# Optimization experiments

Hardware: AMD Instinct MI355X
Metric: run time of the kernel (lower is better)

Reference implementation:

```python
import jax, jax.numpy as jnp
import numpy as np

# MoE config (matches init_kwargs)
E = 32      # num_experts
K = 4       # num_experts_per_tok (top_k)
H = 1024    # hidden_size
I = 512     # moe_intermediate_size (shared expert uses I * num_shared_experts = I)
B, S = 2, 2048
T = B * S
C = 1024
ROUTED_SCALE = 1.0


def _silu_and_mul(gu):
    g, u = jnp.split(gu, 2, axis=-1)
    return jax.nn.silu(g) * u


def setup_inputs() -> dict:
    key = jax.random.key(0)
    ks = jax.random.split(key, 6)
    s = 0.02
    return {
        "hidden_states": jax.random.normal(ks[0], (B, S, H), jnp.float32),
        "gate_w": jax.random.normal(ks[1], (E, H), jnp.float32) * s,
        "w_gate_up": jax.random.normal(ks[2], (E, H, 2 * I), jnp.float32) * s,
        "w_down": jax.random.normal(ks[3], (E, I, H), jnp.float32) * s,
        "shared_w_gate_up": jax.random.normal(ks[4], (H, 2 * I), jnp.float32) * s,
        "shared_w_down": jax.random.normal(ks[5], (I, H), jnp.float32) * s,
    }


def reference(hidden_states, gate_w, w_gate_up, w_down, shared_w_gate_up, shared_w_down):
    b, s, h = hidden_states.shape
    x = hidden_states.reshape(-1, h)                      # [T, H]
    t = x.shape[0]

    # --- router: gate linear -> softmax -> top-k -> renormalize ---
    logits = x @ gate_w.T                                 # [T, E]
    probs = jax.nn.softmax(logits, axis=-1)
    topk_w, topk_idx = jax.lax.top_k(probs, K)            # [T, K]
    topk_w = topk_w / jnp.sum(topk_w, axis=-1, keepdims=True)  # norm_topk_prob
    topk_w = topk_w * ROUTED_SCALE

    # --- dispatch: sort (token, slot) assignments by expert, scatter into capacity buffer ---
    e_flat = topk_idx.reshape(-1)                         # [T*K]
    w_flat = topk_w.reshape(-1)
    t_flat = jnp.repeat(jnp.arange(t), K)
    order = jnp.argsort(e_flat)                           # stable sort by expert id
    e_s, w_s, t_s = e_flat[order], w_flat[order], t_flat[order]
    counts = jax.ops.segment_sum(jnp.ones_like(e_s), e_s, num_segments=E)
    starts = jnp.cumsum(counts) - counts                  # exclusive prefix sum
    pos = jnp.arange(t * K) - starts[e_s]                 # position within expert group
    slot = jnp.minimum(pos, C)                            # overflow -> trash slot C
    buf = jnp.zeros((E, C + 1, h), x.dtype).at[e_s, slot].set(x[t_s])

    # --- grouped expert MLP (silu-gated) ---
    gu = jnp.einsum('ech,ehi->eci', buf[:, :C], w_gate_up)        # [E, C, 2I]
    expert_out = jnp.einsum('eci,eih->ech', _silu_and_mul(gu), w_down)  # [E, C, H]
    expert_out = jnp.pad(expert_out, ((0, 0), (0, 1), (0, 0)))    # trash slot reads zero

    # --- combine: gather back, weight, scatter-add per token ---
    gate = jnp.where(pos < C, w_s, 0.0)[:, None]
    routed = jnp.zeros_like(x).at[t_s].add(expert_out[e_s, slot] * gate)

    # --- shared expert MLP ---
    shared = _silu_and_mul(x @ shared_w_gate_up) @ shared_w_down

    return (routed + shared).reshape(b, s, h)
```

## Files before the change

kernel.cpp:

```cpp
#include <hip/hip_runtime.h>
#include <cstdint>
#include <cstddef>

#define NEXP   32
#define TOPK   4
#define HD     1024
#define ID     512
#define TT     4096
#define CAP    1024
#define SHARED_BASE (NEXP*CAP)
#define NSLOT  (NEXP*CAP + TT)
#define MAXTILES 320

#define KSPLIT 16
#define KCH    64
#define KSUB   16

typedef __attribute__((ext_vector_type(4))) float f32x4;
typedef __bf16 bf16x8 __attribute__((ext_vector_type(8)));

__device__ __forceinline__ unsigned short f2bf(float f) {
    union { float f; unsigned int u; } v; v.f = f;
    unsigned int u = v.u;
    u = (u + 0x7FFFu + ((u >> 16) & 1u)) >> 16;
    return (unsigned short)u;
}
__device__ __forceinline__ float bf2f(unsigned short s) {
    union { unsigned int u; float f; } v; v.u = ((unsigned int)s) << 16;
    return v.f;
}

#define GLOAD_LDS16(g, l)                                                     \
    __builtin_amdgcn_global_load_lds(                                         \
        (__attribute__((address_space(1))) void*)(g),                         \
        (__attribute__((address_space(3))) void*)(l), 16, 0, 0)

__global__ __launch_bounds__(256)
void k_prep(const float* __restrict__ wgu, const float* __restrict__ sgu,
            const float* __restrict__ wdn, const float* __restrict__ sdn,
            unsigned short* __restrict__ wgup_b, unsigned short* __restrict__ wdn_b,
            const float* __restrict__ x, const float* __restrict__ gw,
            float* __restrict__ part, unsigned short* __restrict__ xb) {
    __shared__ __align__(16) char smem[18944];
    const int z = blockIdx.z;
    const int tid = threadIdx.x;

    if (z < 66) {
        const float* s; unsigned short* d;
        const int lb = blockIdx.y * 16 + blockIdx.x;
        if (z < 33) {
            s = (z < NEXP) ? wgu + (size_t)z * (1024 * 1024) : sgu;
            d = wgup_b + (size_t)z * (1024 * 1024);
        } else {
            if (lb >= 128) return;
            int zz = z - 33;
            s = (zz < NEXP) ? wdn + (size_t)zz * (512 * 1024) : sdn;
            d = wdn_b + (size_t)zz * (512 * 1024);
        }
        const size_t base = (size_t)lb * 1024;
#pragma unroll
        for (int j = 0; j < 4; j++) {
            size_t i = base + j * 256 + tid;
            float4 v = ((const float4*)s)[i];
            ushort4 o;
            o.x = f2bf(v.x); o.y = f2bf(v.y); o.z = f2bf(v.z); o.w = f2bf(v.w);
            ((ushort4*)d)[i] = o;
        }
        return;
    }

    float (*xsT)[260] = reinterpret_cast<float(*)[260]>(smem);
    float (*gsT)[36]  = reinterpret_cast<float(*)[36]>(smem + KSUB * 260 * 4);
    const int lane = tid & 63, wv = tid >> 6;
    const int tg = lane >> 2, eg = lane & 3;
    const int t0 = blockIdx.x * 256;
    const int kbase = blockIdx.y * KCH;
    const int tbase = wv * 64 + tg * 4;
    const int ebase = eg * 8;

    float acc[4][8];
#pragma unroll
    for (int j = 0; j < 4; j++)
#pragma unroll
        for (int i = 0; i < 8; i++) acc[j][i] = 0.f;

    for (int ks = 0; ks < KCH; ks += KSUB) {
        const int k0 = kbase + ks;
        if (ks > 0) __syncthreads();
#pragma unroll
        for (int p = 0; p < 4; p++) {
            int vid = p * 256 + tid;
            int t = vid >> 2, kq = (vid & 3) * 4;
            float4 v = *(const float4*)(x + (size_t)(t0 + t) * HD + k0 + kq);
            xsT[kq + 0][t] = v.x; xsT[kq + 1][t] = v.y;
            xsT[kq + 2][t] = v.z; xsT[kq + 3][t] = v.w;
            ushort4 o;
            o.x = f2bf(v.x); o.y = f2bf(v.y); o.z = f2bf(v.z); o.w = f2bf(v.w);
            *(ushort4*)(xb + (size_t)(t0 + t) * HD + k0 + kq) = o;
        }
#pragma unroll
        for (int p = 0; p < 2; p++) {
            int vid = p * 256 + tid;
            int e = vid >> 4, k = vid & 15;
            gsT[k][e] = gw[(size_t)e * HD + k0 + k];
        }
        __syncthreads();
#pragma unroll 4
        for (int k = 0; k < KSUB; k++) {
            float4 xv = *(const float4*)&xsT[k][tbase];
            float4 g0 = *(const float4*)&gsT[k][ebase];
            float4 g1 = *(const float4*)&gsT[k][ebase + 4];
            float xa[4] = {xv.x, xv.y, xv.z, xv.w};
#pragma unroll
            for (int j = 0; j < 4; j++) {
                acc[j][0] += xa[j] * g0.x; acc[j][1] += xa[j] * g0.y;
                acc[j][2] += xa[j] * g0.z; acc[j][3] += xa[j] * g0.w;
                acc[j][4] += xa[j] * g1.x; acc[j][5] += xa[j] * g1.y;
                acc[j][6] += xa[j] * g1.z; acc[j][7] += xa[j] * g1.w;
            }
        }
    }
    const size_t base = ((size_t)blockIdx.y * TT + (t0 + tbase)) * 32 + ebase;
#pragma unroll
    for (int j = 0; j < 4; j++) {
        float4 w0, w1;
        w0.x = acc[j][0]; w0.y = acc[j][1]; w0.z = acc[j][2]; w0.w = acc[j][3];
        w1.x = acc[j][4]; w1.y = acc[j][5]; w1.z = acc[j][6]; w1.w = acc[j][7];
        *(float4*)(part + base + (size_t)j * 32) = w0;
        *(float4*)(part + base + (size_t)j * 32 + 4) = w1;
    }
}

__global__ __launch_bounds__(256)
void k_topk(const float* __restrict__ part,
            int* __restrict__ choice, float* __restrict__ cw,
            int* __restrict__ tok, float* __restrict__ wgt) {
    const int lane = threadIdx.x & 63, wv = threadIdx.x >> 6;
    const int t = blockIdx.x * 4 + wv;
    const int e = lane & 31;
    const int sbase = (lane >> 5) * 8;
    float v = 0.f;
#pragma unroll
    for (int s = 0; s < 8; s++)
        v += part[((size_t)(sbase + s) * TT + t) * 32 + e];
    v += __shfl_xor(v, 32);
    float sc = (lane < 32) ? v : -INFINITY;

    float lv[TOPK]; int le[TOPK];
#pragma unroll
    for (int r = 0; r < TOPK; r++) {
        float m = sc;
#pragma unroll
        for (int d = 1; d < 64; d <<= 1) m = fmaxf(m, __shfl_xor(m, d));
        unsigned long long ball = __ballot(sc == m);
        int widx = __ffsll(ball) - 1;
        lv[r] = m; le[r] = widx;
        if (lane == widx) sc = -INFINITY;
    }
    if (lane == 0) {
        float wv4[TOPK], wsum = 0.f;
#pragma unroll
        for (int r = 0; r < TOPK; r++) { wv4[r] = __expf(lv[r] - lv[0]); wsum += wv4[r]; }
#pragma unroll
        for (int r = 0; r < TOPK; r++) {
            choice[t * TOPK + r] = le[r];
            cw[t * TOPK + r] = wv4[r] / wsum;
        }
        tok[SHARED_BASE + t] = t;
        wgt[SHARED_BASE + t] = 1.0f;
    }
}

__global__ __launch_bounds__(1024)
void k_assign(const int* __restrict__ choice, const float* __restrict__ cw,
              int* __restrict__ cnt, int* __restrict__ tok,
              float* __restrict__ wgt, int* __restrict__ smap) {
    const int e = blockIdx.x;
    const int tid = threadIdx.x, lane = tid & 63, wv = tid >> 6;
    __shared__ int wtot[16];
    int running = 0;
    for (int it = 0; it < TT / 1024; it++) {
        const int t = it * 1024 + tid;
        const int4   c4 = *(const int4*)(choice + t * 4);
        const float4 w4 = *(const float4*)(cw + t * 4);
        unsigned m = (unsigned)(c4.x == e) | ((unsigned)(c4.y == e) << 1)
                   | ((unsigned)(c4.z == e) << 2) | ((unsigned)(c4.w == e) << 3);
        int mc = __popc(m);
        int pre = mc;
#pragma unroll
        for (int d = 1; d < 64; d <<= 1) {
            int up = __shfl_up(pre, d);
            if (lane >= d) pre += up;
        }
        if (lane == 63) wtot[wv] = pre;
        const int wpre = pre - mc;
        __syncthreads();
        int woff = 0, tot = 0;
#pragma unroll
        for (int w = 0; w < 16; w++) { int c = wtot[w]; tot += c; if (w < wv) woff += c; }
        int base = running + woff + wpre;
        running += tot;
        __syncthreads();
        if (m) {
            const float wa[4] = {w4.x, w4.y, w4.z, w4.w};
            int k = 0;
#pragma unroll
            for (int r = 0; r < 4; r++) {
                if (m & (1u << r)) {
                    int pos = base + k;
                    int i = t * 4 + r;
                    if (pos < CAP) {
                        int slot = e * CAP + pos;
                        tok[slot] = t;
                        wgt[slot] = wa[r];
                        smap[i] = slot;
                    } else {
                        smap[i] = -1;
                    }
                    k++;
                }
            }
        }
    }
    if (tid == 0) cnt[e] = min(running, CAP);
}

template <int KD, bool GATHER, bool SILU>
__global__ __launch_bounds__(256)
void k_moe_gemm(const unsigned short* __restrict__ Ab,
                const unsigned short* __restrict__ Bt,
                unsigned short* __restrict__ Cout,
                const int* __restrict__ tok,
                const int* __restrict__ cnt) {
    const int tid  = threadIdx.x;
    const int lane = tid & 63;
    const int wv   = tid >> 6;

    int c_l = (lane < NEXP) ? min(cnt[lane], CAP) : ((lane == NEXP) ? TT : 0);
    int nt_l = (c_l + 127) >> 7;
    int pre = nt_l;
#pragma unroll
    for (int d = 1; d < 64; d <<= 1) {
        int up = __shfl_up(pre, d);
        if (lane >= d) pre += up;
    }
    const int ntl = __shfl(pre, 63);
    const int chunk = (ntl + 7) >> 3;
    const int c_xcd = blockIdx.x;
    const int qy = blockIdx.y;
    if ((qy >> 3) >= chunk) return;
    const int j = c_xcd * chunk + (qy >> 3);
    if (j >= ntl) return;
    const int nt = qy & 7;
    const int start_l = pre - nt_l;
    const bool mine = (j >= start_l) && (j < start_l + nt_l);
    const unsigned long long bl = __ballot(mine);
    const int e_lane = __ffsll((long long)bl) - 1;
    const int e  = e_lane;
    const int mt = j - __shfl(start_l, e_lane);
    const int cE = __shfl(c_l, e_lane);

    const int slotbase = (e < NEXP) ? e * CAP : SHARED_BASE;
    const int m0 = mt * 128;
    const int rowsv = min(128, cE - m0);

    const unsigned short* Bte = Bt + (size_t)e * ((size_t)KD * 1024);

    __shared__ unsigned short As[3][128 * 32];
    __shared__ unsigned short Bs[2][128 * 32];

    const int rr   = lane >> 2;
    const int segA = (lane & 3) ^ ((lane >> 4) & 3);
    const int r0 = wv * 32 + rr;
    const int r1 = r0 + 16;

    int ga0 = m0 + r0, ga1 = m0 + r1;
    int ra0, ra1;
    if (GATHER) {
        ra0 = (ga0 < cE) ? tok[slotbase + ga0] : 0;
        ra1 = (ga1 < cE) ? tok[slotbase + ga1] : 0;
    } else {
        ra0 = slotbase + ga0;
        ra1 = slotbase + ga1;
    }
    const unsigned short* ap0 = Ab + (size_t)ra0 * KD + segA * 8;
    const unsigned short* ap1 = Ab + (size_t)ra1 * KD + segA * 8;
    const int aoff0 = (wv * 32) * 32, aoff1 = (wv * 32 + 16) * 32;

    const int hB = lane >> 5;
    const int nw = lane & 31;
    int rB[4], offB[4];
    int bcol;
    if (SILU) {
        const int sn0 = nw * 4;
        const int side = sn0 >> 6;
        const int jj0 = sn0 & 63;
        bcol = (side ? 512 : 0) + nt * 64 + jj0;
#pragma unroll
        for (int q = 0; q < 4; q++) {
            int jj = jj0 + q;
            rB[q] = ((jj >> 5) << 6) + (side << 5) + (jj & 31);
        }
    } else {
        bcol = nt * 128 + nw * 4;
#pragma unroll
        for (int q = 0; q < 4; q++) rB[q] = nw * 4 + q;
    }
#pragma unroll
    for (int q = 0; q < 4; q++) {
        int slot = wv ^ ((rB[q] >> 2) & 3);
        offB[q] = rB[q] * 32 + slot * 8 + hB * 4;
    }
    const unsigned short* bp = Bte + (size_t)(wv * 8 + hB * 4) * 1024 + bcol;

#define BLOAD(IT, R0, R1, R2, R3)                                             \
    {                                                                         \
        const unsigned short* bpk = bp + (size_t)(IT) * 32 * 1024;            \
        R0 = *(const uint2*)(bpk);                                            \
        R1 = *(const uint2*)(bpk + 1024);                                     \
        R2 = *(const uint2*)(bpk + 2048);                                     \
        R3 = *(const uint2*)(bpk + 3072);                                     \
    }
#define BPACK(BUF, R0, R1, R2, R3)                                            \
    {                                                                         \
        unsigned short* bw = &Bs[BUF][0];                                     \
        _Pragma("unroll")                                                     \
        for (int q = 0; q < 4; q++) {                                         \
            unsigned e0 = ((q < 2 ? R0.x : R0.y) >> (16 * (q & 1))) & 0xffffu;\
            unsigned e1 = ((q < 2 ? R1.x : R1.y) >> (16 * (q & 1))) & 0xffffu;\
            unsigned e2 = ((q < 2 ? R2.x : R2.y) >> (16 * (q & 1))) & 0xffffu;\
            unsigned e3 = ((q < 2 ? R3.x : R3.y) >> (16 * (q & 1))) & 0xffffu;\
            uint2 wv2; wv2.x = e0 | (e1 << 16); wv2.y = e2 | (e3 << 16);      \
            *(uint2*)(bw + offB[q]) = wv2;                                    \
        }                                                                     \
    }

    f32x4 acc[4][4];
#pragma unroll
    for (int i = 0; i < 4; i++)
#pragma unroll
        for (int j2 = 0; j2 < 4; j2++) acc[i][j2] = (f32x4)(0.0f);

    const int mrow = lane & 15;
    const int quad = lane >> 4;
    const int wm = wv >> 1, wn = wv & 1;
    const int sw = (quad ^ ((mrow >> 2) & 3)) * 8;

    const int aRdOff = (wm * 64 + mrow) * 32 + sw;
    const int bRdOff = (wn * 64 + mrow) * 32 + sw;

    uint2 rb0, rb1, rb2, rb3;
    BLOAD(0, rb0, rb1, rb2, rb3);
    __builtin_amdgcn_sched_barrier(0);
    GLOAD_LDS16(ap0, As[0] + aoff0);
    GLOAD_LDS16(ap1, As[0] + aoff1);
    GLOAD_LDS16(ap0 + 32, As[1] + aoff0);
    GLOAD_LDS16(ap1 + 32, As[1] + aoff1);
    __builtin_amdgcn_sched_barrier(0);
    BPACK(0, rb0, rb1, rb2, rb3);

    const int NIT = KD / 32;
    int pA = 0, pB = 0;
    for (int it = 0; it < NIT; ++it) {
        asm volatile("s_waitcnt vmcnt(2) lgkmcnt(0)" ::: "memory");
        __builtin_amdgcn_s_barrier();
        asm volatile("" ::: "memory");

        const bool hasB = (it + 1) < NIT;
        const bool hasA = (it + 2) < NIT;
        if (hasB) BLOAD(it + 1, rb0, rb1, rb2, rb3);
        __builtin_amdgcn_sched_barrier(0);
        if (hasA) {
            int pw = pA + 2; if (pw >= 3) pw -= 3;
            GLOAD_LDS16(ap0 + (it + 2) * 32, As[pw] + aoff0);
            GLOAD_LDS16(ap1 + (it + 2) * 32, As[pw] + aoff1);
        }
        __builtin_amdgcn_sched_barrier(0);

        bf16x8 af[4], bf[4];
#pragma unroll
        for (int i = 0; i < 4; i++) {
            af[i] = *(const bf16x8*)(As[pA] + aRdOff + i * 16 * 32);
            bf[i] = *(const bf16x8*)(Bs[pB] + bRdOff + i * 16 * 32);
        }
#pragma unroll
        for (int mi = 0; mi < 4; mi++)
#pragma unroll
            for (int nj = 0; nj < 4; nj++)
                acc[mi][nj] = __builtin_amdgcn_mfma_f32_16x16x32_bf16(
                    af[mi], bf[nj], acc[mi][nj], 0, 0, 0);
        __builtin_amdgcn_sched_barrier(0);
        if (hasB) BPACK(pB ^ 1, rb0, rb1, rb2, rb3);

        pA++; if (pA >= 3) pA = 0;
        pB ^= 1;
    }
#undef BLOAD
#undef BPACK

    if (SILU) {
#pragma unroll
        for (int mi = 0; mi < 4; mi++)
#pragma unroll
            for (int nj = 0; nj < 2; nj++) {
                f32x4 g = acc[mi][nj];
                f32x4 u = acc[mi][nj + 2];
#pragma unroll
                for (int r = 0; r < 4; r++) {
                    int rloc = wm * 64 + mi * 16 + quad * 4 + r;
                    if (rloc < rowsv) {
                        float gv = g[r], uv = u[r];
                        float a = (gv / (1.f + __expf(-gv))) * uv;
                        int c = nt * 64 + wn * 32 + nj * 16 + mrow;
                        Cout[(size_t)(slotbase + m0 + rloc) * ID + c] = f2bf(a);
                    }
                }
            }
    } else {
#pragma unroll
        for (int mi = 0; mi < 4; mi++)
#pragma unroll
            for (int nj = 0; nj < 4; nj++) {
                f32x4 v = acc[mi][nj];
#pragma unroll
                for (int r = 0; r < 4; r++) {
                    int rloc = wm * 64 + mi * 16 + quad * 4 + r;
                    if (rloc < rowsv) {
                        int c = nt * 128 + wn * 64 + nj * 16 + mrow;
                        Cout[(size_t)(slotbase + m0 + rloc) * HD + c] = f2bf(v[r]);
                    }
                }
            }
    }
}

__global__ __launch_bounds__(256)
void k_combine(const unsigned short* __restrict__ eout,
               const int* __restrict__ smap,
               const float* __restrict__ wgt,
               float* __restrict__ out) {
    const int t = blockIdx.x;
    const int h0 = threadIdx.x * 4;
    ushort4 q = *(const ushort4*)(eout + (size_t)(SHARED_BASE + t) * HD + h0);
    float a0 = bf2f(q.x), a1 = bf2f(q.y), a2 = bf2f(q.z), a3 = bf2f(q.w);
#pragma unroll
    for (int r = 0; r < TOPK; r++) {
        int slot = smap[t * TOPK + r];
        if (slot >= 0) {
            float w = wgt[slot];
            ushort4 e4 = *(const ushort4*)(eout + (size_t)slot * HD + h0);
            a0 += w * bf2f(e4.x); a1 += w * bf2f(e4.y);
            a2 += w * bf2f(e4.z); a3 += w * bf2f(e4.w);
        }
    }
    float4 o; o.x = a0; o.y = a1; o.z = a2; o.w = a3;
    *(float4*)(out + (size_t)t * HD + h0) = o;
}

extern "C" void kernel_launch(void* const* d_in, const int* in_sizes, int n_in,
                              void* d_out, int out_size, void* d_ws, size_t ws_size,
                              hipStream_t stream) {
    const float* x   = (const float*)d_in[0];
    const float* gw  = (const float*)d_in[1];
    const float* wgu = (const float*)d_in[2];
    const float* wdn = (const float*)d_in[3];
    const float* sgu = (const float*)d_in[4];
    const float* sdn = (const float*)d_in[5];
    float* out = (float*)d_out;

    char* w = (char*)d_ws;
    size_t off = 0;
    int* cnt = (int*)(w + off);                       off += 256;
    unsigned short* xb     = (unsigned short*)(w + off); off += (size_t)TT * HD * 2;
    unsigned short* wgup_b = (unsigned short*)(w + off); off += (size_t)33 * 1024 * 1024 * 2;
    unsigned short* wdn_b  = (unsigned short*)(w + off); off += (size_t)33 * 512 * 1024 * 2;
    unsigned short* act    = (unsigned short*)(w + off); off += (size_t)NSLOT * ID * 2;
    int*   tok    = (int*)(w + off);   off += (size_t)NSLOT * 4;
    float* wgt    = (float*)(w + off); off += (size_t)NSLOT * 4;
    int*   smap   = (int*)(w + off);   off += (size_t)TT * TOPK * 4;
    int*   choice = (int*)(w + off);   off += (size_t)TT * TOPK * 4;
    float* cw     = (float*)(w + off); off += (size_t)TT * TOPK * 4;

    float* part = (float*)act;
    unsigned short* eout = xb;

    k_prep<<<dim3(16, 16, 67), 256, 0, stream>>>(wgu, sgu, wdn, sdn,
                                                 wgup_b, wdn_b, x, gw, part, xb);
    k_topk<<<TT / 4, 256, 0, stream>>>(part, choice, cw, tok, wgt);
    k_assign<<<NEXP, 1024, 0, stream>>>(choice, cw, cnt, tok, wgt, smap);

    k_moe_gemm<1024, true, true><<<dim3(8, MAXTILES), 256, 0, stream>>>(xb, wgup_b, act, tok, cnt);
    k_moe_gemm<512, false, false><<<dim3(8, MAXTILES), 256, 0, stream>>>(act, wdn_b, eout, tok, cnt);

    k_combine<<<TT, 256, 0, stream>>>(eout, smap, wgt, out);
}
```

Before: 440.7 us.

## Fuse fp32-to-bf16 weight conversion into MoE GEMM B-tile loads

Removes the separate pass that converts all expert and shared weights to bf16 in a workspace. The grouped GEMMs now read fp32 weights directly and convert them to bf16 with packed convert instructions while staging B tiles into shared memory. This saves writing and re-reading about 100MB of bf16 weights. In exchange, each GEMM tile reads twice as many weight bytes, and weights are re-read per M-tile, which raises global traffic when experts have several tiles. Expert outputs get their own buffer instead of aliasing xb.

```diff
diff --git a/kernel.cpp b/kernel.cpp
--- a/kernel.cpp
+++ b/kernel.cpp
@@ -36,41 +36,11 @@
         (__attribute__((address_space(3))) void*)(l), 16, 0, 0)
 
 __global__ __launch_bounds__(256)
-void k_prep(const float* __restrict__ wgu, const float* __restrict__ sgu,
-            const float* __restrict__ wdn, const float* __restrict__ sdn,
-            unsigned short* __restrict__ wgup_b, unsigned short* __restrict__ wdn_b,
-            const float* __restrict__ x, const float* __restrict__ gw,
-            float* __restrict__ part, unsigned short* __restrict__ xb) {
-    __shared__ __align__(16) char smem[18944];
-    const int z = blockIdx.z;
+void k_logits(const float* __restrict__ x, const float* __restrict__ gw,
+              float* __restrict__ part, unsigned short* __restrict__ xb) {
+    __shared__ float xsT[KSUB][260];
+    __shared__ float gsT[KSUB][36];
     const int tid = threadIdx.x;
-
-    if (z < 66) {
-        const float* s; unsigned short* d;
-        const int lb = blockIdx.y * 16 + blockIdx.x;
-        if (z < 33) {
-            s = (z < NEXP) ? wgu + (size_t)z * (1024 * 1024) : sgu;
-            d = wgup_b + (size_t)z * (1024 * 1024);
-        } else {
-            if (lb >= 128) return;
-            int zz = z - 33;
-            s = (zz < NEXP) ? wdn + (size_t)zz * (512 * 1024) : sdn;
-            d = wdn_b + (size_t)zz * (512 * 1024);
-        }
-        const size_t base = (size_t)lb * 1024;
-#pragma unroll
-        for (int j = 0; j < 4; j++) {
-            size_t i = base + j * 256 + tid;
-            float4 v = ((const float4*)s)[i];
-            ushort4 o;
-            o.x = f2bf(v.x); o.y = f2bf(v.y); o.z = f2bf(v.z); o.w = f2bf(v.w);
-            ((ushort4*)d)[i] = o;
-        }
-        return;
-    }
-
-    float (*xsT)[260] = reinterpret_cast<float(*)[260]>(smem);
-    float (*gsT)[36]  = reinterpret_cast<float(*)[36]>(smem + KSUB * 260 * 4);
     const int lane = tid & 63, wv = tid >> 6;
     const int tg = lane >> 2, eg = lane & 3;
     const int t0 = blockIdx.x * 256;
@@ -228,7 +198,8 @@
 template <int KD, bool GATHER, bool SILU>
 __global__ __launch_bounds__(256)
 void k_moe_gemm(const unsigned short* __restrict__ Ab,
-                const unsigned short* __restrict__ Bt,
+                const float* __restrict__ Bf,
+                const float* __restrict__ BfS,
                 unsigned short* __restrict__ Cout,
                 const int* __restrict__ tok,
                 const int* __restrict__ cnt) {
@@ -264,7 +235,7 @@
     const int m0 = mt * 128;
     const int rowsv = min(128, cE - m0);
 
-    const unsigned short* Bte = Bt + (size_t)e * ((size_t)KD * 1024);
+    const float* Btf = (e < NEXP) ? Bf + (size_t)e * ((size_t)KD * 1024) : BfS;
 
     __shared__ unsigned short As[3][128 * 32];
     __shared__ unsigned short Bs[2][128 * 32];
@@ -311,26 +282,32 @@
         int slot = wv ^ ((rB[q] >> 2) & 3);
         offB[q] = rB[q] * 32 + slot * 8 + hB * 4;
     }
-    const unsigned short* bp = Bte + (size_t)(wv * 8 + hB * 4) * 1024 + bcol;
-
-#define BLOAD(IT, R0, R1, R2, R3)                                             \
+    const float* bpf = Btf + (size_t)(wv * 8 + hB * 4) * 1024 + bcol;
+
+    float4 F0, F1, F2, F3;
+#define BLOAD(IT)                                                             \
     {                                                                         \
-        const unsigned short* bpk = bp + (size_t)(IT) * 32 * 1024;            \
-        R0 = *(const uint2*)(bpk);                                            \
-        R1 = *(const uint2*)(bpk + 1024);                                     \
-        R2 = *(const uint2*)(bpk + 2048);                                     \
-        R3 = *(const uint2*)(bpk + 3072);                                     \
-    }
-#define BPACK(BUF, R0, R1, R2, R3)                                            \
+        const float* bpk = bpf + (size_t)(IT) * 32 * 1024;                    \
+        F0 = *(const float4*)(bpk);                                           \
+        F1 = *(const float4*)(bpk + 1024);                                    \
+        F2 = *(const float4*)(bpk + 2048);                                    \
+        F3 = *(const float4*)(bpk + 3072);                                    \
+    }
+#define BPACK(BUF)                                                            \
     {                                                                         \
         unsigned short* bw = &Bs[BUF][0];                                     \
+        const float* a0p = (const float*)&F0;                                 \
+        const float* a1p = (const float*)&F1;                                 \
+        const float* a2p = (const float*)&F2;                                 \
+        const float* a3p = (const float*)&F3;                                 \
         _Pragma("unroll")                                                     \
         for (int q = 0; q < 4; q++) {                                         \
-            unsigned e0 = ((q < 2 ? R0.x : R0.y) >> (16 * (q & 1))) & 0xffffu;\
-            unsigned e1 = ((q < 2 ? R1.x : R1.y) >> (16 * (q & 1))) & 0xffffu;\
-            unsigned e2 = ((q < 2 ? R2.x : R2.y) >> (16 * (q & 1))) & 0xffffu;\
-            unsigned e3 = ((q < 2 ? R3.x : R3.y) >> (16 * (q & 1))) & 0xffffu;\
-            uint2 wv2; wv2.x = e0 | (e1 << 16); wv2.y = e2 | (e3 << 16);      \
+            unsigned lo, hi;                                                  \
+            asm("v_cvt_pk_bf16_f32 %0, %1, %2"                                \
+                : "=v"(lo) : "v"(a0p[q]), "v"(a1p[q]));                       \
+            asm("v_cvt_pk_bf16_f32 %0, %1, %2"                                \
+                : "=v"(hi) : "v"(a2p[q]), "v"(a3p[q]));                       \
+            uint2 wv2; wv2.x = lo; wv2.y = hi;                                \
             *(uint2*)(bw + offB[q]) = wv2;                                    \
         }                                                                     \
     }
@@ -349,15 +326,14 @@
     const int aRdOff = (wm * 64 + mrow) * 32 + sw;
     const int bRdOff = (wn * 64 + mrow) * 32 + sw;
 
-    uint2 rb0, rb1, rb2, rb3;
-    BLOAD(0, rb0, rb1, rb2, rb3);
+    BLOAD(0);
     __builtin_amdgcn_sched_barrier(0);
     GLOAD_LDS16(ap0, As[0] + aoff0);
     GLOAD_LDS16(ap1, As[0] + aoff1);
     GLOAD_LDS16(ap0 + 32, As[1] + aoff0);
     GLOAD_LDS16(ap1 + 32, As[1] + aoff1);
     __builtin_amdgcn_sched_barrier(0);
-    BPACK(0, rb0, rb1, rb2, rb3);
+    BPACK(0);
 
     const int NIT = KD / 32;
     int pA = 0, pB = 0;
@@ -368,7 +344,7 @@
 
         const bool hasB = (it + 1) < NIT;
         const bool hasA = (it + 2) < NIT;
-        if (hasB) BLOAD(it + 1, rb0, rb1, rb2, rb3);
+        if (hasB) BLOAD(it + 1);
         __builtin_amdgcn_sched_barrier(0);
         if (hasA) {
             int pw = pA + 2; if (pw >= 3) pw -= 3;
@@ -390,7 +366,7 @@
                 acc[mi][nj] = __builtin_amdgcn_mfma_f32_16x16x32_bf16(
                     af[mi], bf[nj], acc[mi][nj], 0, 0, 0);
         __builtin_amdgcn_sched_barrier(0);
-        if (hasB) BPACK(pB ^ 1, rb0, rb1, rb2, rb3);
+        if (hasB) BPACK(pB ^ 1);
 
         pA++; if (pA >= 3) pA = 0;
         pB ^= 1;
@@ -471,10 +447,9 @@
     char* w = (char*)d_ws;
     size_t off = 0;
     int* cnt = (int*)(w + off);                       off += 256;
-    unsigned short* xb     = (unsigned short*)(w + off); off += (size_t)TT * HD * 2;
-    unsigned short* wgup_b = (unsigned short*)(w + off); off += (size_t)33 * 1024 * 1024 * 2;
-    unsigned short* wdn_b  = (unsigned short*)(w + off); off += (size_t)33 * 512 * 1024 * 2;
-    unsigned short* act    = (unsigned short*)(w + off); off += (size_t)NSLOT * ID * 2;
+    unsigned short* xb   = (unsigned short*)(w + off); off += (size_t)TT * HD * 2;
+    unsigned short* act  = (unsigned short*)(w + off); off += (size_t)NSLOT * ID * 2;
+    unsigned short* eout = (unsigned short*)(w + off); off += (size_t)NSLOT * HD * 2;
     int*   tok    = (int*)(w + off);   off += (size_t)NSLOT * 4;
     float* wgt    = (float*)(w + off); off += (size_t)NSLOT * 4;
     int*   smap   = (int*)(w + off);   off += (size_t)TT * TOPK * 4;
@@ -482,15 +457,13 @@
     float* cw     = (float*)(w + off); off += (size_t)TT * TOPK * 4;
 
     float* part = (float*)act;
-    unsigned short* eout = xb;
-
-    k_prep<<<dim3(16, 16, 67), 256, 0, stream>>>(wgu, sgu, wdn, sdn,
-                                                 wgup_b, wdn_b, x, gw, part, xb);
+
+    k_logits<<<dim3(16, KSPLIT), 256, 0, stream>>>(x, gw, part, xb);
     k_topk<<<TT / 4, 256, 0, stream>>>(part, choice, cw, tok, wgt);
     k_assign<<<NEXP, 1024, 0, stream>>>(choice, cw, cnt, tok, wgt, smap);
 
-    k_moe_gemm<1024, true, true><<<dim3(8, MAXTILES), 256, 0, stream>>>(xb, wgup_b, act, tok, cnt);
-    k_moe_gemm<512, false, false><<<dim3(8, MAXTILES), 256, 0, stream>>>(act, wdn_b, eout, tok, cnt);
+    k_moe_gemm<1024, true, true><<<dim3(8, MAXTILES), 256, 0, stream>>>(xb, wgu, sgu, act, tok, cnt);
+    k_moe_gemm<512, false, false><<<dim3(8, MAXTILES), 256, 0, stream>>>(act, wdn, sdn, eout, tok, cnt);
 
     k_combine<<<TT, 256, 0, stream>>>(eout, smap, wgt, out);
 }
```

After: 401.5 us. -8.9%, faster.
